# Optimization experiments

Measured on AMD Instinct MI355X. Metric: run time of the kernel, lower is better.

## Reference

```python
import jax, jax.numpy as jnp
import numpy as np

DIM = 256
NUM_HEADS = 4
HEAD_DIM = DIM // NUM_HEADS
EPS = 1e-5


def setup_inputs() -> dict:
    key = jax.random.key(0)
    ks = jax.random.split(key, 8)
    B, N, C = 8, 2048, DIM
    s = 0.02
    return {
        "x": jax.random.normal(ks[0], (B, N, C), jnp.float32),
        "qkv_w": jax.random.normal(ks[1], (C, 3 * C), jnp.float32) * s,
        "qkv_b": jnp.zeros((3 * C,), jnp.float32),
        "proj_w": jax.random.normal(ks[2], (C, C), jnp.float32) * s,
        "proj_b": jnp.zeros((C,), jnp.float32),
        "ln1_g": jnp.ones((C,), jnp.float32),
        "ln1_b": jnp.zeros((C,), jnp.float32),
        "ln2_g": jnp.ones((C,), jnp.float32),
        "ln2_b": jnp.zeros((C,), jnp.float32),
        "mlp_w1": jax.random.normal(ks[3], (C, 2 * C), jnp.float32) * s,
        "mlp_b1": jnp.zeros((2 * C,), jnp.float32),
        "mlp_w2": jax.random.normal(ks[4], (2 * C, C), jnp.float32) * s,
        "mlp_b2": jnp.zeros((C,), jnp.float32),
    }


def _layernorm(x, g, b):
    mu = jnp.mean(x, axis=-1, keepdims=True)
    var = jnp.mean(jnp.square(x - mu), axis=-1, keepdims=True)
    return (x - mu) * jax.lax.rsqrt(var + EPS) * g + b


def reference(x, qkv_w, qkv_b, proj_w, proj_b, ln1_g, ln1_b, ln2_g, ln2_b,
              mlp_w1, mlp_b1, mlp_w2, mlp_b2):
    B, N, C = x.shape
    H, D = NUM_HEADS, HEAD_DIM
    shortcut = x
    h = _layernorm(x, ln1_g, ln1_b)
    qkv = (h @ qkv_w + qkv_b).reshape(B, N, 3, H, D)
    q = qkv[:, :, 0].transpose(0, 2, 1, 3)  # [B,H,N,D]
    k = qkv[:, :, 1].transpose(0, 2, 1, 3)
    v = qkv[:, :, 2].transpose(0, 2, 1, 3)
    attn = jnp.einsum('bhnd,bhmd->bhnm', q, k) * (D ** -0.5)
    attn = jax.nn.softmax(attn, axis=-1)  # dropout = identity (eval mode)
    o = jnp.einsum('bhnm,bhmd->bhnd', attn, v)
    o = o.transpose(0, 2, 1, 3).reshape(B, N, C)
    x = o @ proj_w + proj_b + shortcut
    h2 = _layernorm(x, ln2_g, ln2_b)
    mlp = jax.nn.gelu(h2 @ mlp_w1 + mlp_b1, approximate=False) @ mlp_w2 + mlp_b2
    return x + mlp
```

## Files before the change

kernel.cpp:

```cpp
#include <hip/hip_runtime.h>

typedef __bf16 bf16;
typedef __bf16 bf16x8 __attribute__((ext_vector_type(8)));
typedef __bf16 bf16x4 __attribute__((ext_vector_type(4)));
typedef float  f32x4  __attribute__((ext_vector_type(4)));
typedef unsigned u32x2 __attribute__((ext_vector_type(2)));

typedef __attribute__((address_space(1))) const void GASV;
typedef __attribute__((address_space(3))) void LASV;

__device__ __forceinline__ void gload16(const void* g, void* l) {
  __builtin_amdgcn_global_load_lds((GASV*)g, (LASV*)l, 16, 0, 0);
}

__global__ __launch_bounds__(256) void wconv_all(const float* __restrict__ qkv_w,
                                                 const float* __restrict__ proj_w,
                                                 const float* __restrict__ w1,
                                                 const float* __restrict__ w2,
                                                 bf16* __restrict__ Wtqkv,
                                                 bf16* __restrict__ WtP,
                                                 bf16* __restrict__ Wt1,
                                                 bf16* __restrict__ Wt2) {
  const int idx = blockIdx.x * 256 + threadIdx.x;
  if (idx < 196608) {
    const int k = idx & 255, n = idx >> 8;
    Wtqkv[idx] = (bf16)qkv_w[k * 768 + n];
  } else if (idx < 262144) {
    const int i = idx - 196608, k = i & 255, n = i >> 8;
    WtP[i] = (bf16)proj_w[k * 256 + n];
  } else if (idx < 393216) {
    const int i = idx - 262144, k = i & 255, n = i >> 8;
    Wt1[i] = (bf16)w1[k * 512 + n];
  } else {
    const int i = idx - 393216, k = i & 511, n = i >> 9;
    Wt2[i] = (bf16)w2[k * 256 + n];
  }
}

__global__ __launch_bounds__(256) void ln_fwd(const float* __restrict__ x,
                                              const float* __restrict__ gam,
                                              const float* __restrict__ bet,
                                              bf16* __restrict__ out) {
  const int lane = threadIdx.x & 63;
  const int w = threadIdx.x >> 6;
  const size_t row = (size_t)blockIdx.x * 4 + w;
  const float4 v = *(const float4*)(x + row * 256 + lane * 4);
  float s1 = v.x + v.y + v.z + v.w;
  float s2 = v.x * v.x + v.y * v.y + v.z * v.z + v.w * v.w;
#pragma unroll
  for (int m = 1; m < 64; m <<= 1) {
    s1 += __shfl_xor(s1, m);
    s2 += __shfl_xor(s2, m);
  }
  const float mu = s1 * (1.0f / 256.0f);
  const float var = s2 * (1.0f / 256.0f) - mu * mu;
  const float rs = rsqrtf(var + 1e-5f);
  const float4 g4 = *(const float4*)(gam + lane * 4);
  const float4 b4 = *(const float4*)(bet + lane * 4);
  bf16x4 o;
  o[0] = (bf16)((v.x - mu) * rs * g4.x + b4.x);
  o[1] = (bf16)((v.y - mu) * rs * g4.y + b4.y);
  o[2] = (bf16)((v.z - mu) * rs * g4.z + b4.z);
  o[3] = (bf16)((v.w - mu) * rs * g4.w + b4.w);
  *(bf16x4*)(out + row * 256 + lane * 4) = o;
}

template <int EPI>
__global__ __launch_bounds__(256) void gemm_bt(const bf16* __restrict__ A,
                                               const bf16* __restrict__ Bt,
                                               const float* __restrict__ bias,
                                               const float* __restrict__ res,
                                               void* __restrict__ outp,
                                               int M, int N, int K) {
  __shared__ bf16 Al[2][8192];
  __shared__ bf16 Bl[2][8192];
  const int tid = threadIdx.x;
  const int lane = tid & 63;
  const int wid = tid >> 6;
  const int wm = wid >> 1, wn = wid & 1;
  const int nbm = M >> 7;
  const int bm = (int)blockIdx.x % nbm;
  const int bn = (int)blockIdx.x / nbm;
  const int m0 = bm << 7, n0 = bn << 7;
  const int nk = K >> 6;

  f32x4 acc[4][4];
#pragma unroll
  for (int i = 0; i < 4; ++i)
#pragma unroll
    for (int j = 0; j < 4; ++j) acc[i][j] = (f32x4){0.f, 0.f, 0.f, 0.f};

  auto stage = [&](int t, int s) {
    const int k0 = t << 6;
#pragma unroll
    for (int p = 0; p < 4; ++p) {
      const int idx = p * 4096 + tid * 16;
      const int row = idx >> 7;
      const int colb = idx & 127;
      gload16((const char*)(A + ((size_t)(m0 + row) * K + k0)) + colb,
              (char*)&Al[s][0] + p * 4096 + ((tid >> 6) << 10));
      gload16((const char*)(Bt + ((size_t)(n0 + row) * K + k0)) + colb,
              (char*)&Bl[s][0] + p * 4096 + ((tid >> 6) << 10));
    }
  };

  stage(0, 0);
  asm volatile("s_waitcnt vmcnt(0)" ::: "memory");
  __syncthreads();

  for (int t = 0; t < nk; ++t) {
    if (t + 1 < nk) stage(t + 1, (t + 1) & 1);
    const bf16* pa = &Al[t & 1][0] + (wm * 64 + (lane & 15)) * 64 + ((lane >> 4) << 3);
    const bf16* pb = &Bl[t & 1][0] + (wn * 64 + (lane & 15)) * 64 + ((lane >> 4) << 3);
    bf16x8 av[4][2], bv[4][2];
#pragma unroll
    for (int f = 0; f < 4; ++f)
#pragma unroll
      for (int ks = 0; ks < 2; ++ks) {
        av[f][ks] = *(const bf16x8*)(pa + f * 1024 + ks * 32);
        bv[f][ks] = *(const bf16x8*)(pb + f * 1024 + ks * 32);
      }
    __builtin_amdgcn_s_setprio(1);
#pragma unroll
    for (int fm = 0; fm < 4; ++fm)
#pragma unroll
      for (int fn = 0; fn < 4; ++fn) {
        acc[fm][fn] = __builtin_amdgcn_mfma_f32_16x16x32_bf16(av[fm][0], bv[fn][0], acc[fm][fn], 0, 0, 0);
        acc[fm][fn] = __builtin_amdgcn_mfma_f32_16x16x32_bf16(av[fm][1], bv[fn][1], acc[fm][fn], 0, 0, 0);
      }
    __builtin_amdgcn_s_setprio(0);
    asm volatile("s_waitcnt vmcnt(0)" ::: "memory");
    __syncthreads();
  }

#pragma unroll
  for (int fm = 0; fm < 4; ++fm)
#pragma unroll
    for (int fn = 0; fn < 4; ++fn) {
      const int r0 = m0 + wm * 64 + fm * 16 + ((lane >> 4) << 2);
      const int c = n0 + wn * 64 + fn * 16 + (lane & 15);
#pragma unroll
      for (int j = 0; j < 4; ++j) {
        const int r = r0 + j;
        const float v = acc[fm][fn][j];
        if constexpr (EPI == 0) {
          ((bf16*)outp)[(size_t)r * N + c] = (bf16)(v + bias[c]);
        } else if constexpr (EPI == 1) {
          ((bf16*)outp)[(size_t)r * 2048 + ((size_t)(c >> 11)) * 524288 + (c & 2047)] =
              (bf16)(v + bias[r]);
        } else if constexpr (EPI == 2) {
          ((float*)outp)[(size_t)r * N + c] = v + bias[c] + res[(size_t)r * N + c];
        } else {
          const float u = v + bias[c];
          ((bf16*)outp)[(size_t)r * N + c] = (bf16)(u * 0.5f * (1.0f + erff(u * 0.70710678118f)));
        }
      }
    }
}

__global__ __launch_bounds__(512, 4) void attn_fwd(const bf16* __restrict__ qk,
                                                   const bf16* __restrict__ vT,
                                                   bf16* __restrict__ ob) {
  __shared__ bf16 Kl[2][2][4096];
  __shared__ bf16 Vl[2][2][4096];
  __shared__ bf16 Pl[8][1024];
  const int tid = threadIdx.x;
  const int lane = tid & 63;
  const int w = tid >> 6;
  const int grp = w >> 2;
  const int wq = w & 3;
  const int g = lane >> 4;
  const int qi = lane & 15;
  const int bh = blockIdx.x & 31;
  const int qt = blockIdx.x >> 5;
  const int b = bh >> 2, h = bh & 3;

  const size_t qrow0 = (size_t)b * 2048 + qt * 128 + wq * 32 + qi;
  bf16x8 qf[2][2];
#pragma unroll
  for (int f = 0; f < 2; ++f) {
    const bf16* qp = qk + (qrow0 + f * 16) * 512 + h * 64 + g * 8;
    qf[f][0] = *(const bf16x8*)qp;
    qf[f][1] = *(const bf16x8*)(qp + 32);
  }

  float mrun[2] = {0.f, 0.f};
  float lsum[2] = {0.f, 0.f};
  f32x4 o[4][2];
#pragma unroll
  for (int i = 0; i < 4; ++i)
#pragma unroll
    for (int f = 0; f < 2; ++f) o[i][f] = (f32x4){0.f, 0.f, 0.f, 0.f};

  constexpr float CEXP = 0.125f * 1.44269504088896340736f;
  constexpr float THR = 8.0f / CEXP;

  const char* kbase = (const char*)qk + ((size_t)b * 2048) * 1024 + 512 + h * 128;
  const char* vbase = (const char*)vT + (size_t)bh * 262144;
  const char* ks[2];
  const char* vs[2];
#pragma unroll
  for (int i = 0; i < 2; ++i) {
    const int fk = i * 2 + (wq >> 1);
    const int half = wq & 1;
    ks[i] = kbase + (size_t)grp * 65536 + (fk * 16 + qi) * 1024 + half * 64 + g * 16;
    vs[i] = vbase + (size_t)grp * 128 + (size_t)(fk * 16 + qi) * 4096 + half * 64 + g * 16;
  }
  char* const kslab = (char*)&Kl[grp][0][0];
  char* const vslab = (char*)&Vl[grp][0][0];
  char* const pw = (char*)&Pl[w][0];
  int paddrb[2];
#pragma unroll
  for (int bb = 0; bb < 2; ++bb)
    paddrb[bb] = (bb * 2 + (g >> 1)) * 256 + qi * 16 + (g & 1) * 8;
  const char* const prd = pw + lane * 16;

  auto stage = [&](int slot) {
    char* kd = kslab + slot * 8192 + wq * 1024;
    char* vd = vslab + slot * 8192 + wq * 1024;
    gload16(ks[0], kd);
    gload16(ks[1], kd + 4096);
    gload16(vs[0], vd);
    gload16(vs[1], vd + 4096);
    ks[0] += 131072; ks[1] += 131072;
    vs[0] += 256;    vs[1] += 256;
  };

  stage(0);
  asm volatile("s_waitcnt vmcnt(0)" ::: "memory");
  __builtin_amdgcn_s_barrier();

  for (int t = 0; t < 16; ++t) {
    if (t < 15) stage((t + 1) & 1);
    const char* kb = kslab + (t & 1) * 8192 + lane * 16;
    f32x4 st[4][2];
    __builtin_amdgcn_s_setprio(1);
#pragma unroll
    for (int fk = 0; fk < 4; ++fk) {
      const bf16x8 k0 = *(const bf16x8*)(kb + fk * 2048);
      const bf16x8 k1 = *(const bf16x8*)(kb + fk * 2048 + 1024);
#pragma unroll
      for (int f = 0; f < 2; ++f) {
        f32x4 z = (f32x4){0.f, 0.f, 0.f, 0.f};
        st[fk][f] = __builtin_amdgcn_mfma_f32_16x16x32_bf16(k0, qf[f][0], z, 0, 0, 0);
        st[fk][f] = __builtin_amdgcn_mfma_f32_16x16x32_bf16(k1, qf[f][1], st[fk][f], 0, 0, 0);
      }
    }
    __builtin_amdgcn_s_setprio(0);
    float pmax[2];
#pragma unroll
    for (int f = 0; f < 2; ++f) {
      float m0 = fmaxf(fmaxf(st[0][f][0], st[0][f][1]), fmaxf(st[0][f][2], st[0][f][3]));
      float m1 = fmaxf(fmaxf(st[1][f][0], st[1][f][1]), fmaxf(st[1][f][2], st[1][f][3]));
      float m2 = fmaxf(fmaxf(st[2][f][0], st[2][f][1]), fmaxf(st[2][f][2], st[2][f][3]));
      float m3 = fmaxf(fmaxf(st[3][f][0], st[3][f][1]), fmaxf(st[3][f][2], st[3][f][3]));
      pmax[f] = fmaxf(fmaxf(m0, m1), fmaxf(m2, m3));
    }
    if (!__all(pmax[0] <= mrun[0] + THR && pmax[1] <= mrun[1] + THR)) {
#pragma unroll
      for (int f = 0; f < 2; ++f) {
        float mt = fmaxf(pmax[f], __shfl_xor(pmax[f], 16));
        mt = fmaxf(mt, __shfl_xor(mt, 32));
        const float mnew = fmaxf(mrun[f], mt);
        const float alpha = exp2f(CEXP * (mrun[f] - mnew));
        lsum[f] *= alpha;
#pragma unroll
        for (int fd = 0; fd < 4; ++fd)
#pragma unroll
          for (int j = 0; j < 4; ++j) o[fd][f][j] *= alpha;
        mrun[f] = mnew;
      }
    }
    unsigned pk[4][2][2];
#pragma unroll
    for (int f = 0; f < 2; ++f) {
      const float negcm = -CEXP * mrun[f];
      float ts = 0.f;
#pragma unroll
      for (int fk = 0; fk < 4; ++fk)
#pragma unroll
        for (int jp = 0; jp < 2; ++jp) {
          const float p0 = exp2f(fmaf(st[fk][f][2 * jp], CEXP, negcm));
          const float p1 = exp2f(fmaf(st[fk][f][2 * jp + 1], CEXP, negcm));
          ts += p0 + p1;
          union { bf16 h2[2]; unsigned u; } cv;
          cv.h2[0] = (bf16)p0;
          cv.h2[1] = (bf16)p1;
          pk[fk][f][jp] = cv.u;
        }
      lsum[f] += ts;
    }
    const char* vb = vslab + (t & 1) * 8192 + lane * 16;
#pragma unroll
    for (int ksl = 0; ksl < 2; ++ksl) {
#pragma unroll
      for (int bb = 0; bb < 2; ++bb) {
        const int fk = 2 * ksl + bb;
#pragma unroll
        for (int f = 0; f < 2; ++f) {
          u32x2 pv2;
          pv2[0] = pk[fk][f][0];
          pv2[1] = pk[fk][f][1];
          *(u32x2*)(pw + f * 1024 + paddrb[bb]) = pv2;
        }
      }
      bf16x8 pa[2];
#pragma unroll
      for (int f = 0; f < 2; ++f) pa[f] = *(const bf16x8*)(prd + f * 1024);
      __builtin_amdgcn_s_setprio(1);
#pragma unroll
      for (int fd = 0; fd < 4; ++fd) {
        const bf16x8 vv = *(const bf16x8*)(vb + fd * 2048 + ksl * 1024);
#pragma unroll
        for (int f = 0; f < 2; ++f)
          o[fd][f] = __builtin_amdgcn_mfma_f32_16x16x32_bf16(vv, pa[f], o[fd][f], 0, 0, 0);
      }
      __builtin_amdgcn_s_setprio(0);
    }
    asm volatile("s_waitcnt vmcnt(0)" ::: "memory");
    __builtin_amdgcn_s_barrier();
  }

#pragma unroll
  for (int f = 0; f < 2; ++f) {
    float l = lsum[f];
    l += __shfl_xor(l, 16);
    l += __shfl_xor(l, 32);
    lsum[f] = l;
  }
  f32x4 stv;
  stv[0] = mrun[0]; stv[1] = lsum[0]; stv[2] = mrun[1]; stv[3] = lsum[1];
  *(f32x4*)((char*)&Pl[0][0] + w * 1024 + lane * 16) = stv;
  char* const oslab = (char*)&Kl[0][0][0] + w * 4096;
#pragma unroll
  for (int fd2 = 0; fd2 < 2; ++fd2) {
    const int wf = grp ? fd2 : 2 + fd2;
#pragma unroll
    for (int f = 0; f < 2; ++f)
      *(f32x4*)(oslab + (fd2 * 2 + f) * 1024 + lane * 16) = o[wf][f];
  }
  __syncthreads();
  const int p = w ^ 4;
  const f32x4 pst = *(const f32x4*)((char*)&Pl[0][0] + p * 1024 + lane * 16);
  const char* const pslab = (char*)&Kl[0][0][0] + p * 4096;
#pragma unroll
  for (int f = 0; f < 2; ++f) {
    const float mme = mrun[f], lme = lsum[f];
    const float mot = pst[2 * f], lot = pst[2 * f + 1];
    const float ms = fmaxf(mme, mot);
    const float am = exp2f(CEXP * (mme - ms));
    const float ao = exp2f(CEXP * (mot - ms));
    const float inv = 1.0f / (lme * am + lot * ao);
#pragma unroll
    for (int fd2 = 0; fd2 < 2; ++fd2) {
      const int kf = grp ? 2 + fd2 : fd2;
      const f32x4 po = *(const f32x4*)(pslab + (fd2 * 2 + f) * 1024 + lane * 16);
      bf16x4 ov;
#pragma unroll
      for (int j = 0; j < 4; ++j)
        ov[j] = (bf16)((o[kf][f][j] * am + po[j] * ao) * inv);
      *(bf16x4*)(ob + (qrow0 + f * 16) * 256 + h * 64 + kf * 16 + g * 4) = ov;
    }
  }
}

extern "C" void kernel_launch(void* const* d_in, const int* in_sizes, int n_in,
                              void* d_out, int out_size, void* d_ws, size_t ws_size,
                              hipStream_t stream) {
  const float* x      = (const float*)d_in[0];
  const float* qkv_w  = (const float*)d_in[1];
  const float* qkv_b  = (const float*)d_in[2];
  const float* proj_w = (const float*)d_in[3];
  const float* proj_b = (const float*)d_in[4];
  const float* ln1_g  = (const float*)d_in[5];
  const float* ln1_b  = (const float*)d_in[6];
  const float* ln2_g  = (const float*)d_in[7];
  const float* ln2_b  = (const float*)d_in[8];
  const float* mlp_w1 = (const float*)d_in[9];
  const float* mlp_b1 = (const float*)d_in[10];
  const float* mlp_w2 = (const float*)d_in[11];
  const float* mlp_b2 = (const float*)d_in[12];
  float* out = (float*)d_out;

  char* ws = (char*)d_ws;
  bf16* Wtqkv = (bf16*)(ws);
  bf16* WtP   = (bf16*)(ws + 393216);
  bf16* Wt1   = (bf16*)(ws + 524288);
  bf16* Wt2   = (bf16*)(ws + 786432);
  bf16* h     = (bf16*)(ws + 1048576);
  bf16* qkb   = (bf16*)(ws + 9437184);
  bf16* vT    = (bf16*)(ws + 26214400);
  bf16* obuf  = (bf16*)(ws + 34603008);
  float* x2   = (float*)(ws + 42991616);
  bf16* a1 = qkb;
  bf16* h2 = h;

  wconv_all<<<2048, 256, 0, stream>>>(qkv_w, proj_w, mlp_w1, mlp_w2, Wtqkv, WtP, Wt1, Wt2);

  ln_fwd<<<4096, 256, 0, stream>>>(x, ln1_g, ln1_b, h);
  gemm_bt<0><<<512, 256, 0, stream>>>(h, Wtqkv, qkv_b, nullptr, qkb, 16384, 512, 256);
  gemm_bt<1><<<256, 256, 0, stream>>>(Wtqkv + 512 * 256, h, qkv_b + 512, nullptr, vT, 256, 16384, 256);
  attn_fwd<<<512, 512, 0, stream>>>(qkb, vT, obuf);
  gemm_bt<2><<<256, 256, 0, stream>>>(obuf, WtP, proj_b, x, x2, 16384, 256, 256);
  ln_fwd<<<4096, 256, 0, stream>>>(x2, ln2_g, ln2_b, h2);
  gemm_bt<3><<<512, 256, 0, stream>>>(h2, Wt1, mlp_b1, nullptr, a1, 16384, 512, 256);
  gemm_bt<2><<<256, 256, 0, stream>>>(a1, Wt2, mlp_b2, x2, out, 16384, 256, 512);
}
```

Measured before the change: 198.0 us.

## Split attention KV range across blocks with separate merge kernel

Replaces the in-block two-group split-K attention (512 threads, LDS merge) with 1024 independent 256-thread blocks, each handling half of the key range. Each block writes unnormalized partial outputs in bf16 plus per-row max/sum stats to workspace, and a new merge kernel combines the two halves. The aim is more, smaller blocks for better occupancy and scheduling. The cost is an extra launch, extra global traffic for partials, and bf16 rounding of the unnormalized partials.

```diff
diff --git a/kernel.cpp b/kernel.cpp
--- a/kernel.cpp
+++ b/kernel.cpp
@@ -12,6 +12,8 @@
 __device__ __forceinline__ void gload16(const void* g, void* l) {
   __builtin_amdgcn_global_load_lds((GASV*)g, (LASV*)l, 16, 0, 0);
 }
+
+constexpr float CEXP = 0.125f * 1.44269504088896340736f;
 
 __global__ __launch_bounds__(256) void wconv_all(const float* __restrict__ qkv_w,
                                                  const float* __restrict__ proj_w,
@@ -158,24 +160,25 @@
     }
 }
 
-__global__ __launch_bounds__(512, 4) void attn_fwd(const bf16* __restrict__ qk,
-                                                   const bf16* __restrict__ vT,
-                                                   bf16* __restrict__ ob) {
-  __shared__ bf16 Kl[2][2][4096];
-  __shared__ bf16 Vl[2][2][4096];
-  __shared__ bf16 Pl[8][1024];
+__global__ __launch_bounds__(256) void attn_fwd(const bf16* __restrict__ qk,
+                                                const bf16* __restrict__ vT,
+                                                bf16* __restrict__ po,
+                                                float* __restrict__ pstats) {
+  __shared__ bf16 Kl[2][4096];
+  __shared__ bf16 Vl[2][4096];
+  __shared__ bf16 Pl[4][1024];
   const int tid = threadIdx.x;
   const int lane = tid & 63;
   const int w = tid >> 6;
-  const int grp = w >> 2;
-  const int wq = w & 3;
   const int g = lane >> 4;
   const int qi = lane & 15;
-  const int bh = blockIdx.x & 31;
-  const int qt = blockIdx.x >> 5;
+  const int bid = (int)blockIdx.x;
+  const int bh = bid & 31;
+  const int qt = (bid >> 5) & 15;
+  const int s = bid >> 9;
   const int b = bh >> 2, h = bh & 3;
 
-  const size_t qrow0 = (size_t)b * 2048 + qt * 128 + wq * 32 + qi;
+  const size_t qrow0 = (size_t)b * 2048 + qt * 128 + w * 32 + qi;
   bf16x8 qf[2][2];
 #pragma unroll
   for (int f = 0; f < 2; ++f) {
@@ -192,22 +195,20 @@
 #pragma unroll
     for (int f = 0; f < 2; ++f) o[i][f] = (f32x4){0.f, 0.f, 0.f, 0.f};
 
-  constexpr float CEXP = 0.125f * 1.44269504088896340736f;
   constexpr float THR = 8.0f / CEXP;
 
-  const char* kbase = (const char*)qk + ((size_t)b * 2048) * 1024 + 512 + h * 128;
-  const char* vbase = (const char*)vT + (size_t)bh * 262144;
+  const char* kbase = (const char*)qk + ((size_t)b * 2048) * 1024 + 512 + h * 128 +
+                      (size_t)s * 16 * 65536;
+  const char* vbase = (const char*)vT + (size_t)bh * 262144 + (size_t)s * 16 * 128;
   const char* ks[2];
   const char* vs[2];
 #pragma unroll
   for (int i = 0; i < 2; ++i) {
-    const int fk = i * 2 + (wq >> 1);
-    const int half = wq & 1;
-    ks[i] = kbase + (size_t)grp * 65536 + (fk * 16 + qi) * 1024 + half * 64 + g * 16;
-    vs[i] = vbase + (size_t)grp * 128 + (size_t)(fk * 16 + qi) * 4096 + half * 64 + g * 16;
-  }
-  char* const kslab = (char*)&Kl[grp][0][0];
-  char* const vslab = (char*)&Vl[grp][0][0];
+    const int fk = i * 2 + (w >> 1);
+    const int half = w & 1;
+    ks[i] = kbase + (fk * 16 + qi) * 1024 + half * 64 + g * 16;
+    vs[i] = vbase + (size_t)(fk * 16 + qi) * 4096 + half * 64 + g * 16;
+  }
   char* const pw = (char*)&Pl[w][0];
   int paddrb[2];
 #pragma unroll
@@ -216,14 +217,14 @@
   const char* const prd = pw + lane * 16;
 
   auto stage = [&](int slot) {
-    char* kd = kslab + slot * 8192 + wq * 1024;
-    char* vd = vslab + slot * 8192 + wq * 1024;
+    char* kd = (char*)&Kl[0][0] + slot * 8192 + w * 1024;
+    char* vd = (char*)&Vl[0][0] + slot * 8192 + w * 1024;
     gload16(ks[0], kd);
     gload16(ks[1], kd + 4096);
     gload16(vs[0], vd);
     gload16(vs[1], vd + 4096);
-    ks[0] += 131072; ks[1] += 131072;
-    vs[0] += 256;    vs[1] += 256;
+    ks[0] += 65536; ks[1] += 65536;
+    vs[0] += 128;   vs[1] += 128;
   };
 
   stage(0);
@@ -232,7 +233,7 @@
 
   for (int t = 0; t < 16; ++t) {
     if (t < 15) stage((t + 1) & 1);
-    const char* kb = kslab + (t & 1) * 8192 + lane * 16;
+    const char* kb = (const char*)&Kl[0][0] + (t & 1) * 8192 + lane * 16;
     f32x4 st[4][2];
     __builtin_amdgcn_s_setprio(1);
 #pragma unroll
@@ -290,7 +291,7 @@
         }
       lsum[f] += ts;
     }
-    const char* vb = vslab + (t & 1) * 8192 + lane * 16;
+    const char* vb = (const char*)&Vl[0][0] + (t & 1) * 8192 + lane * 16;
 #pragma unroll
     for (int ksl = 0; ksl < 2; ++ksl) {
 #pragma unroll
@@ -328,40 +329,50 @@
     l += __shfl_xor(l, 32);
     lsum[f] = l;
   }
-  f32x4 stv;
-  stv[0] = mrun[0]; stv[1] = lsum[0]; stv[2] = mrun[1]; stv[3] = lsum[1];
-  *(f32x4*)((char*)&Pl[0][0] + w * 1024 + lane * 16) = stv;
-  char* const oslab = (char*)&Kl[0][0][0] + w * 4096;
-#pragma unroll
-  for (int fd2 = 0; fd2 < 2; ++fd2) {
-    const int wf = grp ? fd2 : 2 + fd2;
-#pragma unroll
-    for (int f = 0; f < 2; ++f)
-      *(f32x4*)(oslab + (fd2 * 2 + f) * 1024 + lane * 16) = o[wf][f];
-  }
-  __syncthreads();
-  const int p = w ^ 4;
-  const f32x4 pst = *(const f32x4*)((char*)&Pl[0][0] + p * 1024 + lane * 16);
-  const char* const pslab = (char*)&Kl[0][0][0] + p * 4096;
+  if (g == 0) {
+#pragma unroll
+    for (int f = 0; f < 2; ++f) {
+      float2 sv;
+      sv.x = mrun[f];
+      sv.y = lsum[f];
+      *(float2*)(pstats + (((size_t)s * 32 + bh) * 2048 + qt * 128 + w * 32 + f * 16 + qi) * 2) = sv;
+    }
+  }
 #pragma unroll
   for (int f = 0; f < 2; ++f) {
-    const float mme = mrun[f], lme = lsum[f];
-    const float mot = pst[2 * f], lot = pst[2 * f + 1];
-    const float ms = fmaxf(mme, mot);
-    const float am = exp2f(CEXP * (mme - ms));
-    const float ao = exp2f(CEXP * (mot - ms));
-    const float inv = 1.0f / (lme * am + lot * ao);
-#pragma unroll
-    for (int fd2 = 0; fd2 < 2; ++fd2) {
-      const int kf = grp ? 2 + fd2 : fd2;
-      const f32x4 po = *(const f32x4*)(pslab + (fd2 * 2 + f) * 1024 + lane * 16);
+    bf16* const orow = po + ((size_t)s * 16384 + qrow0 + f * 16) * 256 + h * 64 + g * 4;
+#pragma unroll
+    for (int fd = 0; fd < 4; ++fd) {
       bf16x4 ov;
 #pragma unroll
-      for (int j = 0; j < 4; ++j)
-        ov[j] = (bf16)((o[kf][f][j] * am + po[j] * ao) * inv);
-      *(bf16x4*)(ob + (qrow0 + f * 16) * 256 + h * 64 + kf * 16 + g * 4) = ov;
-    }
-  }
+      for (int j = 0; j < 4; ++j) ov[j] = (bf16)o[fd][f][j];
+      *(bf16x4*)(orow + fd * 16) = ov;
+    }
+  }
+}
+
+__global__ __launch_bounds__(256) void attn_merge(const bf16* __restrict__ po,
+                                                  const float* __restrict__ pstats,
+                                                  bf16* __restrict__ ob) {
+  const int idx = blockIdx.x * 256 + threadIdx.x;
+  const int r = idx >> 6;
+  const int cq = (idx & 63) * 4;
+  const int h = cq >> 6;
+  const int bh = (r >> 11) * 4 + h;
+  const int ql = r & 2047;
+  const float2 s0 = *(const float2*)(pstats + (((size_t)bh) * 2048 + ql) * 2);
+  const float2 s1 = *(const float2*)(pstats + (((size_t)32 + bh) * 2048 + ql) * 2);
+  const float M = fmaxf(s0.x, s1.x);
+  const float a0 = exp2f(CEXP * (s0.x - M));
+  const float a1 = exp2f(CEXP * (s1.x - M));
+  const float inv = 1.0f / (s0.y * a0 + s1.y * a1);
+  const bf16x4 p0 = *(const bf16x4*)(po + (size_t)r * 256 + cq);
+  const bf16x4 p1 = *(const bf16x4*)(po + ((size_t)16384 + r) * 256 + cq);
+  bf16x4 ov;
+#pragma unroll
+  for (int j = 0; j < 4; ++j)
+    ov[j] = (bf16)(((float)p0[j] * a0 + (float)p1[j] * a1) * inv);
+  *(bf16x4*)(ob + (size_t)r * 256 + cq) = ov;
 }
 
 extern "C" void kernel_launch(void* const* d_in, const int* in_sizes, int n_in,
@@ -392,6 +403,8 @@
   bf16* vT    = (bf16*)(ws + 26214400);
   bf16* obuf  = (bf16*)(ws + 34603008);
   float* x2   = (float*)(ws + 42991616);
+  bf16* po    = (bf16*)(ws + 42991616);
+  float* pstats = (float*)(ws + 59768832);
   bf16* a1 = qkb;
   bf16* h2 = h;
 
@@ -400,7 +413,8 @@
   ln_fwd<<<4096, 256, 0, stream>>>(x, ln1_g, ln1_b, h);
   gemm_bt<0><<<512, 256, 0, stream>>>(h, Wtqkv, qkv_b, nullptr, qkb, 16384, 512, 256);
   gemm_bt<1><<<256, 256, 0, stream>>>(Wtqkv + 512 * 256, h, qkv_b + 512, nullptr, vT, 256, 16384, 256);
-  attn_fwd<<<512, 512, 0, stream>>>(qkb, vT, obuf);
+  attn_fwd<<<1024, 256, 0, stream>>>(qkb, vT, po, pstats);
+  attn_merge<<<4096, 256, 0, stream>>>(po, pstats, obuf);
   gemm_bt<2><<<256, 256, 0, stream>>>(obuf, WtP, proj_b, x, x2, 16384, 256, 256);
   ln_fwd<<<4096, 256, 0, stream>>>(x2, ln2_g, ln2_b, h2);
   gemm_bt<3><<<512, 256, 0, stream>>>(h2, Wt1, mlp_b1, nullptr, a1, 16384, 512, 256);
```

Result: faster. 175.4 us (-11.4%).
